# Kernel optimization log

Measured on AMD Instinct MI355X. Metric: run time of the kernel, lower is better.

Reference implementation:

```python
import jax, jax.numpy as jnp
import numpy as np

ALPHA = 1.702
LIMIT = 7.0


def setup_inputs() -> dict:
    key = jax.random.key(0)
    ks = jax.random.split(key, 6)
    T, H, D, E = 8192, 1024, 1024, 8
    hidden_states = jax.random.normal(ks[0], (T, H), dtype=jnp.float32)
    routing_weights = jax.random.uniform(ks[1], (T, E), dtype=jnp.float32)
    # 0.02 scale keeps activations in a sane range (original uses raw randn params)
    gate_up_proj = jax.random.normal(ks[2], (E, H, 2 * D), dtype=jnp.float32) * 0.02
    gate_up_proj_bias = jax.random.normal(ks[3], (E, 2 * D), dtype=jnp.float32) * 0.02
    down_proj = jax.random.normal(ks[4], (E, D, H), dtype=jnp.float32) * 0.02
    down_proj_bias = jax.random.normal(ks[5], (E, H), dtype=jnp.float32) * 0.02
    return {
        "hidden_states": hidden_states,
        "routing_weights": routing_weights,
        "gate_up_proj": gate_up_proj,
        "gate_up_proj_bias": gate_up_proj_bias,
        "down_proj": down_proj,
        "down_proj_bias": down_proj_bias,
    }


def reference(hidden_states, routing_weights, gate_up_proj, gate_up_proj_bias,
              down_proj, down_proj_bias):
    # hidden_states: [T, H]; routing_weights: [T, E] (batch_size == T in the torch code)
    B, H = hidden_states.shape[0], hidden_states.shape[-1]
    hs = hidden_states.reshape(-1, H)  # [T, H]
    # all-experts batched GEMM: [E, T, 2D]
    gate_up = jnp.einsum('th,ehd->etd', hs, gate_up_proj) + gate_up_proj_bias[:, None, :]
    gate = jnp.minimum(gate_up[..., ::2], LIMIT)          # [E, T, D]
    up = jnp.clip(gate_up[..., 1::2], -LIMIT, LIMIT)      # [E, T, D]
    glu = gate * jax.nn.sigmoid(gate * ALPHA)
    # down projection: [E, T, H]
    next_states = jnp.einsum('etd,edh->eth', (up + 1.0) * glu, down_proj) \
        + down_proj_bias[:, None, :]
    # routing-weighted combine over experts: [T, H]
    out = jnp.einsum('eth,te->th', next_states, routing_weights)
    return out.reshape(B, -1, H)  # [T, 1, H], matching final .view(batch_size, -1, hidden)
```

## Files before the change

### kernel.cpp

```cpp
#include <hip/hip_runtime.h>
#include <hip/hip_bf16.h>

#define T_DIM 8192
#define H_DIM 1024
#define D_DIM 1024
#define E_DIM 8
#define TWO_D 2048
#define K2 8192

#define ALPHA_C 1.702f
#define LIMIT_C 7.0f

typedef __attribute__((ext_vector_type(8))) short s8v;
typedef __attribute__((ext_vector_type(4))) float f4v;

__device__ __forceinline__ void g2l16(const void* g, void* l) {
    __builtin_amdgcn_global_load_lds((const __attribute__((address_space(1))) void*)g,
                                     (__attribute__((address_space(3))) void*)l, 16, 0, 0);
}

__device__ __forceinline__ unsigned short f2bf(float f) {
    __hip_bfloat16 h = __float2bfloat16(f);
    return __builtin_bit_cast(unsigned short, h);
}


__global__ void f32_to_bf16_kernel(const float* __restrict__ in,
                                   unsigned short* __restrict__ out, size_t n) {
    size_t i = ((size_t)blockIdx.x * blockDim.x + threadIdx.x) * 4;
    if (i + 3 < n) {
        float4 v = *(const float4*)(in + i);
        ushort4 o;
        o.x = f2bf(v.x); o.y = f2bf(v.y); o.z = f2bf(v.z); o.w = f2bf(v.w);
        *(ushort4*)(out + i) = o;
    }
}

__global__ void transpose_conv_kernel(const float* __restrict__ in,
                                      unsigned short* __restrict__ out,
                                      int cols, size_t ibs, size_t obs, size_t ors,
                                      int remap) {
    __shared__ float t[32][33];
    const int b = blockIdx.z;
    const int c0 = blockIdx.x * 32, r0 = blockIdx.y * 32;
    const int tx = threadIdx.x & 31, ty = threadIdx.x >> 5;
    const float* ip = in + (size_t)b * ibs;
    #pragma unroll
    for (int i = 0; i < 4; ++i)
        t[ty + i * 8][tx] = ip[(size_t)(r0 + ty + i * 8) * cols + c0 + tx];
    __syncthreads();
    unsigned short* op = out + (size_t)b * obs;
    #pragma unroll
    for (int i = 0; i < 4; ++i) {
        int c = c0 + ty + i * 8;
        int nc = remap ? ((c & ~31) + ((c & 1) << 4) + ((c >> 1) & 15)) : c;
        op[(size_t)nc * ors + r0 + tx] = f2bf(t[tx][ty + i * 8]);
    }
}

__global__ void transpose_w3_tiled_kernel(const float* __restrict__ in,
                                          unsigned short* __restrict__ out) {
    __shared__ float t[32][33];
    const int e = blockIdx.z;
    const int c0 = blockIdx.x * 32;
    const int r0 = blockIdx.y * 32;
    const int tx = threadIdx.x & 31, ty = threadIdx.x >> 5;
    const float* ip = in + (size_t)e * D_DIM * H_DIM;
    #pragma unroll
    for (int i = 0; i < 4; ++i)
        t[ty + i * 8][tx] = ip[(size_t)(r0 + ty + i * 8) * H_DIM + c0 + tx];
    __syncthreads();
    #pragma unroll
    for (int i = 0; i < 4; ++i) {
        const int hcol = c0 + ty + i * 8;
        const int kk = e * D_DIM + r0 + tx;
        const int nt = hcol >> 7, rIn = hcol & 127;
        const int kt = kk >> 6, c = kk & 63;
        out[((size_t)nt * 128 + kt) * 8192 + rIn * 64 + (c ^ ((rIn & 7) << 3))] =
            f2bf(t[tx][ty + i * 8]);
    }
}

__global__ void reduce_bias_kernel(const float* __restrict__ p0f,
                                   const float* __restrict__ rw,
                                   const float* __restrict__ b3,
                                   float* __restrict__ out) {
    const int t = blockIdx.x;
    const int h = threadIdx.x * 4;
    const size_t idx = (size_t)t * H_DIM + h;
    float r[E_DIM];
    #pragma unroll
    for (int e = 0; e < E_DIM; ++e) r[e] = rw[(size_t)t * E_DIM + e];
    float4 v = *(const float4*)(out + idx);
    float4 p = *(const float4*)(p0f + idx);
    v.x += p.x; v.y += p.y; v.z += p.z; v.w += p.w;
    #pragma unroll
    for (int e = 0; e < E_DIM; ++e) {
        float4 bb = *(const float4*)(b3 + (size_t)e * H_DIM + h);
        v.x += r[e] * bb.x; v.y += r[e] * bb.y; v.z += r[e] * bb.z; v.w += r[e] * bb.w;
    }
    *(float4*)(out + idx) = v;
}


__global__ __launch_bounds__(256, 2) void gemm1_kernel(
    const short* __restrict__ Ag0,
    const short* __restrict__ Bg0,
    const float* __restrict__ b1,
    const float* __restrict__ rw,
    unsigned short* __restrict__ act2t)
{
    const int e = blockIdx.z;
    const int mBase = blockIdx.x * 128;
    const int nBase = blockIdx.y * 128;
    const int tid = threadIdx.x;
    const int lane = tid & 63;
    const int wave = tid >> 6;
    const int wm = wave >> 1, wn = wave & 1;
    const int cq = lane & 15, quad = lane >> 4;

    __shared__ __align__(16) short As[128 * 64];
    __shared__ __align__(16) short Bs[128 * 64];

    const short* Ag = Ag0 + (size_t)mBase * H_DIM;
    const short* Bg = Bg0 + ((size_t)e * TWO_D + nBase) * H_DIM;

    f4v acc[4][4];
    #pragma unroll
    for (int mt = 0; mt < 4; ++mt)
        #pragma unroll
        for (int nt = 0; nt < 4; ++nt)
            acc[mt][nt] = (f4v){0.f, 0.f, 0.f, 0.f};

    const int srow8 = lane >> 3;
    const int gco = ((lane & 7) ^ srow8) * 8;
    const int cq7 = cq & 7;

    for (int k0 = 0; k0 < H_DIM; k0 += 64) {
        #pragma unroll
        for (int i = 0; i < 4; ++i) {
            const int r = wave * 32 + i * 8 + srow8;
            g2l16(Ag + (size_t)r * H_DIM + k0 + gco, As + (wave * 32 + i * 8) * 64);
            g2l16(Bg + (size_t)r * H_DIM + k0 + gco, Bs + (wave * 32 + i * 8) * 64);
        }
        __syncthreads();
        #pragma unroll
        for (int h = 0; h < 2; ++h) {
            s8v af[4], bf[4];
            const int pc = (((h << 2) + quad) ^ cq7) * 8;
            #pragma unroll
            for (int i = 0; i < 4; ++i) {
                af[i] = *(const s8v*)(As + (wm * 64 + i * 16 + cq) * 64 + pc);
                bf[i] = *(const s8v*)(Bs + (wn * 64 + i * 16 + cq) * 64 + pc);
            }
            #pragma unroll
            for (int mt = 0; mt < 4; ++mt)
                #pragma unroll
                for (int nt = 0; nt < 4; ++nt)
                    acc[mt][nt] = __builtin_amdgcn_mfma_f32_16x16x32_bf16(
                        af[mt], bf[nt], acc[mt][nt], 0, 0, 0);
        }
        __syncthreads();
    }

    float rwv[4][4];
    #pragma unroll
    for (int mt = 0; mt < 4; ++mt)
        #pragma unroll
        for (int r = 0; r < 4; ++r)
            rwv[mt][r] = rw[(size_t)(mBase + wm * 64 + mt * 16 + quad * 4 + r) * E_DIM + e];

    const int kt_blk = e * 16 + blockIdx.y;
    unsigned short* tb = act2t + ((size_t)blockIdx.x * 128 + kt_blk) * 8192;

    #pragma unroll
    for (int p = 0; p < 2; ++p) {
        const int j = (((nBase + wn * 64 + p * 32) >> 5) << 4) + cq;
        const float gb = b1[(size_t)e * TWO_D + 2 * j];
        const float ub = b1[(size_t)e * TWO_D + 2 * j + 1];
        const int c = wn * 32 + p * 16 + cq;
        #pragma unroll
        for (int mt = 0; mt < 4; ++mt) {
            #pragma unroll
            for (int r = 0; r < 4; ++r) {
                float gate = acc[mt][2 * p][r] + gb;
                float up   = acc[mt][2 * p + 1][r] + ub;
                gate = fminf(gate, LIMIT_C);
                up = fminf(fmaxf(up, -LIMIT_C), LIMIT_C);
                float glu = gate / (1.f + __expf(-ALPHA_C * gate));
                float a = (up + 1.f) * glu * rwv[mt][r];
                const int rIn = wm * 64 + mt * 16 + quad * 4 + r;
                tb[rIn * 64 + (c ^ ((rIn & 7) << 3))] = f2bf(a);
            }
        }
    }
}


__global__ __launch_bounds__(256, 2) void gemm2_kernel(
    const short* __restrict__ At,
    const short* __restrict__ Bt,
    float* __restrict__ out,
    float* __restrict__ p0f)
{
    const int id = blockIdx.x;
    const int mIdx = id & 31;
    const int nIdx = (id >> 5) & 7;
    const int ks = id >> 8;
    const int tid = threadIdx.x;
    const int lane = tid & 63;
    const int wave = tid >> 6;
    const int wm = wave >> 1, wn = wave & 1;
    const int cq = lane & 15, quad = lane >> 4;
    const int cq7 = cq & 7;
    const int lane8 = lane * 8;

    __shared__ __align__(16) short As[256 * 64];
    __shared__ __align__(16) short Bs[128 * 64];

    f4v acc[8][4];
    #pragma unroll
    for (int mt = 0; mt < 8; ++mt)
        #pragma unroll
        for (int nt = 0; nt < 4; ++nt)
            acc[mt][nt] = (f4v){0.f, 0.f, 0.f, 0.f};

    #pragma unroll 1
    for (int s = 0; s < 64; ++s) {
        const int kt = ks * 64 + s;
        #pragma unroll
        for (int i = 0; i < 8; ++i) {
            const int R = i * 32 + wave * 8;
            const short* src = At +
                ((size_t)(2 * mIdx + (R >> 7)) * 128 + kt) * 8192 + (R & 127) * 64 + lane8;
            g2l16(src, As + R * 64);
        }
        #pragma unroll
        for (int i = 0; i < 4; ++i) {
            const int R = i * 32 + wave * 8;
            const short* src = Bt + ((size_t)nIdx * 128 + kt) * 8192 + R * 64 + lane8;
            g2l16(src, Bs + R * 64);
        }
        __syncthreads();
        #pragma unroll
        for (int h = 0; h < 2; ++h) {
            const int pc = (((h << 2) + quad) ^ cq7) * 8;
            s8v bf[4];
            #pragma unroll
            for (int i = 0; i < 4; ++i)
                bf[i] = *(const s8v*)(Bs + (wn * 64 + i * 16 + cq) * 64 + pc);
            #pragma unroll
            for (int mt = 0; mt < 8; ++mt) {
                const s8v af = *(const s8v*)(As + (wm * 128 + mt * 16 + cq) * 64 + pc);
                #pragma unroll
                for (int nt = 0; nt < 4; ++nt)
                    acc[mt][nt] = __builtin_amdgcn_mfma_f32_16x16x32_bf16(
                        af, bf[nt], acc[mt][nt], 0, 0, 0);
            }
        }
        __syncthreads();
    }

    float* dst = (ks == 0) ? out : p0f;
    const int mBase = mIdx * 256;
    const int nBase = nIdx * 128;
    #pragma unroll
    for (int mt = 0; mt < 8; ++mt) {
        #pragma unroll
        for (int r = 0; r < 4; ++r) {
            const int row = mBase + wm * 128 + mt * 16 + quad * 4 + r;
            #pragma unroll
            for (int nt = 0; nt < 4; ++nt) {
                const int col = nBase + wn * 64 + nt * 16 + cq;
                dst[(size_t)row * H_DIM + col] = acc[mt][nt][r];
            }
        }
    }
}


extern "C" void kernel_launch(void* const* d_in, const int* in_sizes, int n_in,
                              void* d_out, int out_size, void* d_ws, size_t ws_size,
                              hipStream_t stream) {
    const float* hs = (const float*)d_in[0];
    const float* rw = (const float*)d_in[1];
    const float* w1 = (const float*)d_in[2];
    const float* b1 = (const float*)d_in[3];
    const float* w3 = (const float*)d_in[4];
    const float* b3 = (const float*)d_in[5];
    float* out = (float*)d_out;

    char* ws = (char*)d_ws;
    unsigned short* hsb   = (unsigned short*)(ws);
    unsigned short* w1b   = (unsigned short*)(ws + ((size_t)16 << 20));
    unsigned short* w3t   = (unsigned short*)(ws + ((size_t)48 << 20));
    unsigned short* act2t = (unsigned short*)(ws + ((size_t)64 << 20));
    float* p0f = (float*)(ws);

    {
        size_t n = (size_t)T_DIM * H_DIM;
        f32_to_bf16_kernel<<<dim3(n / (256 * 4)), dim3(256), 0, stream>>>(hs, hsb, n);
    }
    transpose_conv_kernel<<<dim3(TWO_D / 32, H_DIM / 32, E_DIM), dim3(256), 0, stream>>>(
        w1, w1b, TWO_D, (size_t)H_DIM * TWO_D, (size_t)TWO_D * H_DIM, (size_t)H_DIM, 1);
    transpose_w3_tiled_kernel<<<dim3(H_DIM / 32, D_DIM / 32, E_DIM), dim3(256), 0, stream>>>(
        w3, w3t);
    gemm1_kernel<<<dim3(T_DIM / 128, TWO_D / 128, E_DIM), dim3(256), 0, stream>>>(
        (const short*)hsb, (const short*)w1b, b1, rw, act2t);
    gemm2_kernel<<<dim3(512), dim3(256), 0, stream>>>(
        (const short*)act2t, (const short*)w3t, out, p0f);
    reduce_bias_kernel<<<dim3(T_DIM), dim3(H_DIM / 4), 0, stream>>>(
        p0f, rw, b3, out);
}
```

Baseline: 559.2 us.

## Double-buffer A tile in gemm2 to prefetch next k-step during MFMA

The gemm2 kernel now keeps two LDS buffers for the A tile. It issues the global-to-LDS loads for step s+1 before computing step s, and waits with an explicit vmcnt(8) so only the current B and A loads must land before the barrier. The MFMA section also runs at raised wave priority through s_setprio. This is meant to hide global load latency behind matrix work. In exchange, LDS use rises by 32KB per block, which may hurt occupancy at 2 blocks per CU, and the B tile is still single-buffered.

```diff
diff --git a/kernel.cpp b/kernel.cpp
--- a/kernel.cpp
+++ b/kernel.cpp
@@ -23,6 +23,9 @@
     __hip_bfloat16 h = __float2bfloat16(f);
     return __builtin_bit_cast(unsigned short, h);
 }
+
+#define FEN asm volatile("" ::: "memory")
+#define BARR { FEN; __builtin_amdgcn_s_barrier(); FEN; }
 
 
 __global__ void f32_to_bf16_kernel(const float* __restrict__ in,
@@ -215,7 +218,7 @@
     const int cq7 = cq & 7;
     const int lane8 = lane * 8;
 
-    __shared__ __align__(16) short As[256 * 64];
+    __shared__ __align__(16) short As[2][256 * 64];
     __shared__ __align__(16) short Bs[128 * 64];
 
     f4v acc[8][4];
@@ -225,40 +228,62 @@
         for (int nt = 0; nt < 4; ++nt)
             acc[mt][nt] = (f4v){0.f, 0.f, 0.f, 0.f};
 
+#define STG_A(T, BUF)                                                             \
+    { const int _kt = ks * 64 + (T);                                              \
+      _Pragma("unroll")                                                           \
+      for (int i = 0; i < 8; ++i) {                                               \
+          const int R = i * 32 + wave * 8;                                        \
+          const short* _src = At +                                                \
+              ((size_t)(2 * mIdx + (R >> 7)) * 128 + _kt) * 8192                  \
+              + (R & 127) * 64 + lane8;                                           \
+          g2l16(_src, &As[BUF][R * 64]);                                          \
+      } }
+#define STG_B(T)                                                                  \
+    { const int _kt = ks * 64 + (T);                                              \
+      _Pragma("unroll")                                                           \
+      for (int i = 0; i < 4; ++i) {                                               \
+          const int R = i * 32 + wave * 8;                                        \
+          const short* _src = Bt + ((size_t)nIdx * 128 + _kt) * 8192              \
+                            + R * 64 + lane8;                                     \
+          g2l16(_src, &Bs[R * 64]);                                               \
+      } }
+
+    STG_A(0, 0);
+
+    int cur = 0;
     #pragma unroll 1
     for (int s = 0; s < 64; ++s) {
-        const int kt = ks * 64 + s;
-        #pragma unroll
-        for (int i = 0; i < 8; ++i) {
-            const int R = i * 32 + wave * 8;
-            const short* src = At +
-                ((size_t)(2 * mIdx + (R >> 7)) * 128 + kt) * 8192 + (R & 127) * 64 + lane8;
-            g2l16(src, As + R * 64);
-        }
-        #pragma unroll
-        for (int i = 0; i < 4; ++i) {
-            const int R = i * 32 + wave * 8;
-            const short* src = Bt + ((size_t)nIdx * 128 + kt) * 8192 + R * 64 + lane8;
-            g2l16(src, Bs + R * 64);
-        }
-        __syncthreads();
-        #pragma unroll
-        for (int h = 0; h < 2; ++h) {
-            const int pc = (((h << 2) + quad) ^ cq7) * 8;
-            s8v bf[4];
-            #pragma unroll
-            for (int i = 0; i < 4; ++i)
-                bf[i] = *(const s8v*)(Bs + (wn * 64 + i * 16 + cq) * 64 + pc);
-            #pragma unroll
-            for (int mt = 0; mt < 8; ++mt) {
-                const s8v af = *(const s8v*)(As + (wm * 128 + mt * 16 + cq) * 64 + pc);
+        STG_B(s);
+        if (s + 1 < 64) {
+            STG_A(s + 1, cur ^ 1);
+            asm volatile("s_waitcnt vmcnt(8)" ::: "memory");
+        } else {
+            asm volatile("s_waitcnt vmcnt(0)" ::: "memory");
+        }
+        BARR;
+        {
+            const short* Ab = As[cur];
+            __builtin_amdgcn_s_setprio(1);
+            #pragma unroll
+            for (int h = 0; h < 2; ++h) {
+                const int pc = (((h << 2) + quad) ^ cq7) * 8;
+                s8v bf[4];
                 #pragma unroll
-                for (int nt = 0; nt < 4; ++nt)
-                    acc[mt][nt] = __builtin_amdgcn_mfma_f32_16x16x32_bf16(
-                        af, bf[nt], acc[mt][nt], 0, 0, 0);
+                for (int i = 0; i < 4; ++i)
+                    bf[i] = *(const s8v*)(Bs + (wn * 64 + i * 16 + cq) * 64 + pc);
+                #pragma unroll
+                for (int mt = 0; mt < 8; ++mt) {
+                    const s8v af = *(const s8v*)(Ab + (wm * 128 + mt * 16 + cq) * 64 + pc);
+                    #pragma unroll
+                    for (int nt = 0; nt < 4; ++nt)
+                        acc[mt][nt] = __builtin_amdgcn_mfma_f32_16x16x32_bf16(
+                            af, bf[nt], acc[mt][nt], 0, 0, 0);
+                }
             }
-        }
-        __syncthreads();
+            __builtin_amdgcn_s_setprio(0);
+        }
+        BARR;
+        cur ^= 1;
     }
 
     float* dst = (ks == 0) ? out : p0f;
```

Measured after the change: 571.2 us. +2.2%, slower.
